# Performance work log

Measured on AMD Instinct MI355X. Metric: run time of the kernel, lower is better.

The kernel has to match this reference:

```python
import jax, jax.numpy as jnp
import numpy as np

B, N, DIM, H = 4, 1024, 384, 12
EPS = 1e-6


def setup_inputs() -> dict:
    key = jax.random.key(0)
    ks = jax.random.split(key, 5)
    return {
        "x": jax.random.normal(ks[0], (B, N, DIM), dtype=jnp.float32),
        "w_qkv": jax.random.normal(ks[1], (DIM, 3 * DIM), dtype=jnp.float32) * 0.05,
        "w_out": jax.random.normal(ks[2], (DIM, DIM), dtype=jnp.float32) * 0.05,
        "b_out": jax.random.normal(ks[3], (DIM,), dtype=jnp.float32) * 0.05,
        "toeplitz_w": jax.random.normal(ks[4], (2 * N - 1,), dtype=jnp.float32),
    }


def reference(x, w_qkv, w_out, b_out, toeplitz_w):
    b, n, c = x.shape
    d = c // H
    qkv = x @ w_qkv                                   # [B,N,3C]
    q, k, v = jnp.split(qkv, 3, axis=-1)
    def heads(t):
        return t.reshape(b, n, H, d).transpose(0, 2, 1, 3)  # [B,H,N,d]
    q, k, v = heads(q), heads(k), heads(v)
    q = jax.nn.relu(q) + EPS
    k = jax.nn.relu(k) + EPS
    # outer product kv signal: [B,H,N,d,d]
    kv = k[..., :, None] * v[..., None, :]
    kv_flat = kv.reshape(b * H, n, d * d)
    k_flat = k.reshape(b * H, n, d)
    combined = jnp.concatenate([kv_flat, k_flat], axis=-1)   # [BH,N,d^2+d]
    fft_len = 2 * n
    sig_f = jnp.fft.rfft(combined, n=fft_len, axis=1)        # [BH,N+1,d^2+d] complex
    w_pad = jnp.zeros(fft_len, dtype=x.dtype).at[: 2 * n - 1].set(toeplitz_w)
    w_rolled = jnp.roll(w_pad, -(n - 1))
    w_f = jnp.fft.rfft(w_rolled, n=fft_len)                  # [N+1]
    out_f = sig_f * w_f[None, :, None]
    out_t = jnp.fft.irfft(out_f, n=fft_len, axis=1)[:, :n, :]  # [BH,N,d^2+d]
    kv_conv = out_t[:, :, : d * d].reshape(b, H, n, d, d)
    k_conv = out_t[:, :, d * d:].reshape(b, H, n, d)
    num = jnp.einsum('bhnd,bhndc->bhnc', q, kv_conv)
    den = jnp.einsum('bhnd,bhnd->bhn', q, k_conv)[..., None] + EPS
    out = (num / den).transpose(0, 2, 1, 3).reshape(b, n, c)
    return out @ w_out.T + b_out
```

## Files before the change

kernel.cpp:

```cpp
#include <hip/hip_runtime.h>

#define EPS 1e-6f


__global__ __launch_bounds__(256) void qkv_gemm(const float* __restrict__ x,
                                                const float* __restrict__ w,
                                                float* __restrict__ qw,
                                                float* __restrict__ kw,
                                                float* __restrict__ vw) {
    __shared__ float As[16][132];
    __shared__ float Bs[16][128];
    const int t = threadIdx.x;
    const int m0 = blockIdx.y * 128;
    const int c0 = blockIdx.x * 128;
    const int tx = t & 15, ty = t >> 4;

    float acc[8][8];
#pragma unroll
    for (int i = 0; i < 8; i++)
#pragma unroll
        for (int j = 0; j < 8; j++) acc[i][j] = 0.f;

    for (int k0 = 0; k0 < 384; k0 += 16) {
        __syncthreads();
#pragma unroll
        for (int l = 0; l < 2; l++) {
            int idx = t * 2 + l;
            int r = idx >> 2, c4 = (idx & 3) * 4;
            float4 a = *(const float4*)(x + (size_t)(m0 + r) * 384 + k0 + c4);
            As[c4 + 0][r] = a.x;
            As[c4 + 1][r] = a.y;
            As[c4 + 2][r] = a.z;
            As[c4 + 3][r] = a.w;
        }
#pragma unroll
        for (int l = 0; l < 2; l++) {
            int idx = t * 2 + l;
            int kr = idx >> 5, cc = (idx & 31) * 4;
            *(float4*)&Bs[kr][cc] = *(const float4*)(w + (size_t)(k0 + kr) * 1152 + c0 + cc);
        }
        __syncthreads();
#pragma unroll
        for (int kk = 0; kk < 16; kk++) {
            float4 a0 = *(float4*)&As[kk][ty * 8];
            float4 a1 = *(float4*)&As[kk][ty * 8 + 4];
            float4 b0 = *(float4*)&Bs[kk][tx * 8];
            float4 b1 = *(float4*)&Bs[kk][tx * 8 + 4];
            float av[8] = {a0.x, a0.y, a0.z, a0.w, a1.x, a1.y, a1.z, a1.w};
            float bv[8] = {b0.x, b0.y, b0.z, b0.w, b1.x, b1.y, b1.z, b1.w};
#pragma unroll
            for (int i = 0; i < 8; i++)
#pragma unroll
                for (int j = 0; j < 8; j++) acc[i][j] += av[i] * bv[j];
        }
    }
#pragma unroll
    for (int i = 0; i < 8; i++) {
        int row = m0 + ty * 8 + i;
        int b = row >> 10, n = row & 1023;
#pragma unroll
        for (int j = 0; j < 8; j++) {
            int col = c0 + tx * 8 + j;
            float vv = acc[i][j];
            float* dst;
            int cc;
            if (col < 384) { dst = qw; cc = col; vv = fmaxf(vv, 0.f) + EPS; }
            else if (col < 768) { dst = kw; cc = col - 384; vv = fmaxf(vv, 0.f) + EPS; }
            else { dst = vw; cc = col - 768; }
            int h = cc >> 5, dd = cc & 31;
            dst[(size_t)((b * 12 + h) * 1024 + n) * 32 + dd] = vv;
        }
    }
}

__global__ __launch_bounds__(256) void toep_attn(const float* __restrict__ q,
                                                 const float* __restrict__ k,
                                                 const float* __restrict__ v,
                                                 const float* __restrict__ tw,
                                                 float* __restrict__ op) {
    const int t = threadIdx.x;
    const int n0 = blockIdx.x * 64;
    const int bh = blockIdx.y;
    const int b = bh / 12, h = bh % 12;
    __shared__ float Qt[32][68];
    __shared__ float Kt[32][68];
    __shared__ float Vs[64][32];
    __shared__ float Ss[64][68];
    __shared__ float Ts[128];

    const float* qb = q + (size_t)bh * 1024 * 32;
    const float* kb = k + (size_t)bh * 1024 * 32;
    const float* vb = v + (size_t)bh * 1024 * 32;

#pragma unroll
    for (int l = 0; l < 2; l++) {
        int idx = t * 2 + l;
        int r = idx >> 3, c4 = (idx & 7) * 4;
        float4 a = *(const float4*)(qb + (size_t)(n0 + r) * 32 + c4);
        Qt[c4 + 0][r] = a.x;
        Qt[c4 + 1][r] = a.y;
        Qt[c4 + 2][r] = a.z;
        Qt[c4 + 3][r] = a.w;
    }

    const int sx = t & 15, sy = t >> 4;
    const int pr = t >> 2;
    const int pc = (t & 3) * 8;
    double num[8] = {0, 0, 0, 0, 0, 0, 0, 0};
    double den = 0.0;

    for (int m0 = 0; m0 < 1024; m0 += 64) {
        __syncthreads();
#pragma unroll
        for (int l = 0; l < 2; l++) {
            int idx = t * 2 + l;
            int r = idx >> 3, c4 = (idx & 7) * 4;
            float4 a = *(const float4*)(kb + (size_t)(m0 + r) * 32 + c4);
            Kt[c4 + 0][r] = a.x;
            Kt[c4 + 1][r] = a.y;
            Kt[c4 + 2][r] = a.z;
            Kt[c4 + 3][r] = a.w;
            ((float4*)&Vs[0][0])[idx] = *(const float4*)(vb + (size_t)m0 * 32 + idx * 4);
        }
        if (t < 127) Ts[t] = tw[n0 - m0 + 960 + t];
        __syncthreads();

        float acc[4][4];
#pragma unroll
        for (int i = 0; i < 4; i++)
#pragma unroll
            for (int j = 0; j < 4; j++) acc[i][j] = 0.f;
#pragma unroll
        for (int kk = 0; kk < 32; kk++) {
            float4 a = *(float4*)&Qt[kk][sy * 4];
            float4 bb = *(float4*)&Kt[kk][sx * 4];
            float av[4] = {a.x, a.y, a.z, a.w};
            float bv[4] = {bb.x, bb.y, bb.z, bb.w};
#pragma unroll
            for (int i = 0; i < 4; i++)
#pragma unroll
                for (int j = 0; j < 4; j++) acc[i][j] += av[i] * bv[j];
        }
#pragma unroll
        for (int i = 0; i < 4; i++) {
            int r = sy * 4 + i;
            float4 srow;
            srow.x = acc[i][0] * Ts[r - sx * 4 + 63];
            srow.y = acc[i][1] * Ts[r - sx * 4 + 62];
            srow.z = acc[i][2] * Ts[r - sx * 4 + 61];
            srow.w = acc[i][3] * Ts[r - sx * 4 + 60];
            *(float4*)&Ss[r][sx * 4] = srow;
        }
        __syncthreads();

#pragma unroll 4
        for (int m = 0; m < 64; m++) {
            double s = (double)Ss[pr][m];
            float4 v0 = *(float4*)&Vs[m][pc];
            float4 v1 = *(float4*)&Vs[m][pc + 4];
            den += s;
            num[0] += s * (double)v0.x; num[1] += s * (double)v0.y;
            num[2] += s * (double)v0.z; num[3] += s * (double)v0.w;
            num[4] += s * (double)v1.x; num[5] += s * (double)v1.y;
            num[6] += s * (double)v1.z; num[7] += s * (double)v1.w;
        }
    }
    double inv = 1.0 / (den + (double)EPS);
    float* o = op + (size_t)((b * 1024) + n0 + pr) * 384 + h * 32 + pc;
    float4 o0 = {(float)(num[0] * inv), (float)(num[1] * inv),
                 (float)(num[2] * inv), (float)(num[3] * inv)};
    float4 o1 = {(float)(num[4] * inv), (float)(num[5] * inv),
                 (float)(num[6] * inv), (float)(num[7] * inv)};
    *(float4*)o = o0;
    *(float4*)(o + 4) = o1;
}

__global__ __launch_bounds__(256) void out_gemm(const float* __restrict__ a,
                                                const float* __restrict__ w,
                                                const float* __restrict__ bias,
                                                float* __restrict__ out) {
    __shared__ float As[16][132];
    __shared__ float Bs[16][132];
    const int t = threadIdx.x;
    const int m0 = blockIdx.y * 128;
    const int c0 = blockIdx.x * 128;
    const int tx = t & 15, ty = t >> 4;

    float acc[8][8];
#pragma unroll
    for (int i = 0; i < 8; i++)
#pragma unroll
        for (int j = 0; j < 8; j++) acc[i][j] = 0.f;

    for (int k0 = 0; k0 < 384; k0 += 16) {
        __syncthreads();
#pragma unroll
        for (int l = 0; l < 2; l++) {
            int idx = t * 2 + l;
            int r = idx >> 2, c4 = (idx & 3) * 4;
            float4 av = *(const float4*)(a + (size_t)(m0 + r) * 384 + k0 + c4);
            As[c4 + 0][r] = av.x;
            As[c4 + 1][r] = av.y;
            As[c4 + 2][r] = av.z;
            As[c4 + 3][r] = av.w;
        }
#pragma unroll
        for (int l = 0; l < 2; l++) {
            int idx = t * 2 + l;
            int r = idx >> 2, c4 = (idx & 3) * 4;
            float4 wv = *(const float4*)(w + (size_t)(c0 + r) * 384 + k0 + c4);
            Bs[c4 + 0][r] = wv.x;
            Bs[c4 + 1][r] = wv.y;
            Bs[c4 + 2][r] = wv.z;
            Bs[c4 + 3][r] = wv.w;
        }
        __syncthreads();
#pragma unroll
        for (int kk = 0; kk < 16; kk++) {
            float4 a0 = *(float4*)&As[kk][ty * 8];
            float4 a1 = *(float4*)&As[kk][ty * 8 + 4];
            float4 b0 = *(float4*)&Bs[kk][tx * 8];
            float4 b1 = *(float4*)&Bs[kk][tx * 8 + 4];
            float av[8] = {a0.x, a0.y, a0.z, a0.w, a1.x, a1.y, a1.z, a1.w};
            float bv[8] = {b0.x, b0.y, b0.z, b0.w, b1.x, b1.y, b1.z, b1.w};
#pragma unroll
            for (int i = 0; i < 8; i++)
#pragma unroll
                for (int j = 0; j < 8; j++) acc[i][j] += av[i] * bv[j];
        }
    }
#pragma unroll
    for (int i = 0; i < 8; i++) {
        int row = m0 + ty * 8 + i;
#pragma unroll
        for (int j = 0; j < 8; j++) {
            int col = c0 + tx * 8 + j;
            out[(size_t)row * 384 + col] = acc[i][j] + bias[col];
        }
    }
}

extern "C" void kernel_launch(void* const* d_in, const int* in_sizes, int n_in,
                              void* d_out, int out_size, void* d_ws, size_t ws_size,
                              hipStream_t stream) {
    const float* x     = (const float*)d_in[0];
    const float* w_qkv = (const float*)d_in[1];
    const float* w_out = (const float*)d_in[2];
    const float* b_out = (const float*)d_in[3];
    const float* tw    = (const float*)d_in[4];
    float* out = (float*)d_out;

    float* qw = (float*)d_ws;
    float* kw = qw + 1572864;
    float* vw = kw + 1572864;
    float* op = vw + 1572864;

    qkv_gemm<<<dim3(9, 32), 256, 0, stream>>>(x, w_qkv, qw, kw, vw);
    toep_attn<<<dim3(16, 48), 256, 0, stream>>>(qw, kw, vw, tw, op);
    out_gemm<<<dim3(3, 32), 256, 0, stream>>>(op, w_out, b_out, out);
}
```

Measured before the change: 367.2 us.

## Shrink GEMM tiles, vectorize epilogues, prefetch K/V and pre-convert V to double

```diff
diff --git a/kernel.cpp b/kernel.cpp
--- a/kernel.cpp
+++ b/kernel.cpp
@@ -8,25 +8,25 @@
                                                 float* __restrict__ qw,
                                                 float* __restrict__ kw,
                                                 float* __restrict__ vw) {
-    __shared__ float As[16][132];
-    __shared__ float Bs[16][128];
+    __shared__ float As[32][68];
+    __shared__ float Bs[32][68];
     const int t = threadIdx.x;
-    const int m0 = blockIdx.y * 128;
-    const int c0 = blockIdx.x * 128;
+    const int m0 = blockIdx.y * 64;
+    const int c0 = blockIdx.x * 64;
     const int tx = t & 15, ty = t >> 4;
 
-    float acc[8][8];
-#pragma unroll
-    for (int i = 0; i < 8; i++)
-#pragma unroll
-        for (int j = 0; j < 8; j++) acc[i][j] = 0.f;
-
-    for (int k0 = 0; k0 < 384; k0 += 16) {
+    float acc[4][4];
+#pragma unroll
+    for (int i = 0; i < 4; i++)
+#pragma unroll
+        for (int j = 0; j < 4; j++) acc[i][j] = 0.f;
+
+    for (int k0 = 0; k0 < 384; k0 += 32) {
         __syncthreads();
 #pragma unroll
         for (int l = 0; l < 2; l++) {
             int idx = t * 2 + l;
-            int r = idx >> 2, c4 = (idx & 3) * 4;
+            int r = idx >> 3, c4 = (idx & 7) * 4;
             float4 a = *(const float4*)(x + (size_t)(m0 + r) * 384 + k0 + c4);
             As[c4 + 0][r] = a.x;
             As[c4 + 1][r] = a.y;
@@ -36,40 +36,40 @@
 #pragma unroll
         for (int l = 0; l < 2; l++) {
             int idx = t * 2 + l;
-            int kr = idx >> 5, cc = (idx & 31) * 4;
+            int kr = idx >> 4, cc = (idx & 15) * 4;
             *(float4*)&Bs[kr][cc] = *(const float4*)(w + (size_t)(k0 + kr) * 1152 + c0 + cc);
         }
         __syncthreads();
 #pragma unroll
-        for (int kk = 0; kk < 16; kk++) {
-            float4 a0 = *(float4*)&As[kk][ty * 8];
-            float4 a1 = *(float4*)&As[kk][ty * 8 + 4];
-            float4 b0 = *(float4*)&Bs[kk][tx * 8];
-            float4 b1 = *(float4*)&Bs[kk][tx * 8 + 4];
-            float av[8] = {a0.x, a0.y, a0.z, a0.w, a1.x, a1.y, a1.z, a1.w};
-            float bv[8] = {b0.x, b0.y, b0.z, b0.w, b1.x, b1.y, b1.z, b1.w};
-#pragma unroll
-            for (int i = 0; i < 8; i++)
-#pragma unroll
-                for (int j = 0; j < 8; j++) acc[i][j] += av[i] * bv[j];
-        }
-    }
-#pragma unroll
-    for (int i = 0; i < 8; i++) {
-        int row = m0 + ty * 8 + i;
+        for (int kk = 0; kk < 32; kk++) {
+            float4 a = *(float4*)&As[kk][ty * 4];
+            float4 bb = *(float4*)&Bs[kk][tx * 4];
+            float av[4] = {a.x, a.y, a.z, a.w};
+            float bv[4] = {bb.x, bb.y, bb.z, bb.w};
+#pragma unroll
+            for (int i = 0; i < 4; i++)
+#pragma unroll
+                for (int j = 0; j < 4; j++) acc[i][j] += av[i] * bv[j];
+        }
+    }
+    const int sec = (c0 + tx * 4) / 384;
+    float* dst = (sec == 0) ? qw : (sec == 1) ? kw : vw;
+    const int cc0 = c0 + tx * 4 - sec * 384;
+    const int h = cc0 >> 5, dd = cc0 & 31;
+#pragma unroll
+    for (int i = 0; i < 4; i++) {
+        int row = m0 + ty * 4 + i;
         int b = row >> 10, n = row & 1023;
-#pragma unroll
-        for (int j = 0; j < 8; j++) {
-            int col = c0 + tx * 8 + j;
-            float vv = acc[i][j];
-            float* dst;
-            int cc;
-            if (col < 384) { dst = qw; cc = col; vv = fmaxf(vv, 0.f) + EPS; }
-            else if (col < 768) { dst = kw; cc = col - 384; vv = fmaxf(vv, 0.f) + EPS; }
-            else { dst = vw; cc = col - 768; }
-            int h = cc >> 5, dd = cc & 31;
-            dst[(size_t)((b * 12 + h) * 1024 + n) * 32 + dd] = vv;
-        }
+        float4 o;
+        if (sec < 2) {
+            o.x = fmaxf(acc[i][0], 0.f) + EPS;
+            o.y = fmaxf(acc[i][1], 0.f) + EPS;
+            o.z = fmaxf(acc[i][2], 0.f) + EPS;
+            o.w = fmaxf(acc[i][3], 0.f) + EPS;
+        } else {
+            o = make_float4(acc[i][0], acc[i][1], acc[i][2], acc[i][3]);
+        }
+        *(float4*)(dst + (size_t)((b * 12 + h) * 1024 + n) * 32 + dd) = o;
     }
 }
 
@@ -84,13 +84,13 @@
     const int b = bh / 12, h = bh % 12;
     __shared__ float Qt[32][68];
     __shared__ float Kt[32][68];
-    __shared__ float Vs[64][32];
+    __shared__ double Vd[64][32];
     __shared__ float Ss[64][68];
     __shared__ float Ts[128];
 
-    const float* qb = q + (size_t)bh * 1024 * 32;
-    const float* kb = k + (size_t)bh * 1024 * 32;
-    const float* vb = v + (size_t)bh * 1024 * 32;
+    const float* qb = q + (size_t)bh * 32768;
+    const float* kb = k + (size_t)bh * 32768;
+    const float* vb = v + (size_t)bh * 32768;
 
 #pragma unroll
     for (int l = 0; l < 2; l++) {
@@ -103,27 +103,47 @@
         Qt[c4 + 3][r] = a.w;
     }
 
+    float4 kreg[2], vreg[2];
+#pragma unroll
+    for (int l = 0; l < 2; l++) {
+        int idx = t * 2 + l;
+        int r = idx >> 3, c4 = (idx & 7) * 4;
+        kreg[l] = *(const float4*)(kb + (size_t)r * 32 + c4);
+        vreg[l] = *(const float4*)(vb + idx * 4);
+    }
+#pragma unroll
+    for (int l = 0; l < 2; l++) {
+        int idx = t * 2 + l;
+        int r = idx >> 3, c4 = (idx & 7) * 4;
+        Kt[c4 + 0][r] = kreg[l].x;
+        Kt[c4 + 1][r] = kreg[l].y;
+        Kt[c4 + 2][r] = kreg[l].z;
+        Kt[c4 + 3][r] = kreg[l].w;
+        double2 d0 = {(double)vreg[l].x, (double)vreg[l].y};
+        double2 d1 = {(double)vreg[l].z, (double)vreg[l].w};
+        *(double2*)&Vd[r][c4] = d0;
+        *(double2*)&Vd[r][c4 + 2] = d1;
+    }
+    if (t < 127) Ts[t] = tw[n0 + 960 + t];
+    __syncthreads();
+
     const int sx = t & 15, sy = t >> 4;
     const int pr = t >> 2;
     const int pc = (t & 3) * 8;
     double num[8] = {0, 0, 0, 0, 0, 0, 0, 0};
     double den = 0.0;
 
-    for (int m0 = 0; m0 < 1024; m0 += 64) {
-        __syncthreads();
-#pragma unroll
-        for (int l = 0; l < 2; l++) {
-            int idx = t * 2 + l;
-            int r = idx >> 3, c4 = (idx & 7) * 4;
-            float4 a = *(const float4*)(kb + (size_t)(m0 + r) * 32 + c4);
-            Kt[c4 + 0][r] = a.x;
-            Kt[c4 + 1][r] = a.y;
-            Kt[c4 + 2][r] = a.z;
-            Kt[c4 + 3][r] = a.w;
-            ((float4*)&Vs[0][0])[idx] = *(const float4*)(vb + (size_t)m0 * 32 + idx * 4);
-        }
-        if (t < 127) Ts[t] = tw[n0 - m0 + 960 + t];
-        __syncthreads();
+    for (int tt = 0; tt < 16; tt++) {
+        const int m0 = tt * 64;
+        if (tt < 15) {
+#pragma unroll
+            for (int l = 0; l < 2; l++) {
+                int idx = t * 2 + l;
+                int r = idx >> 3, c4 = (idx & 7) * 4;
+                kreg[l] = *(const float4*)(kb + (size_t)(m0 + 64 + r) * 32 + c4);
+                vreg[l] = *(const float4*)(vb + (size_t)(m0 + 64) * 32 + idx * 4);
+            }
+        }
 
         float acc[4][4];
 #pragma unroll
@@ -153,16 +173,43 @@
         }
         __syncthreads();
 
+        if (tt < 15) {
+#pragma unroll
+            for (int l = 0; l < 2; l++) {
+                int idx = t * 2 + l;
+                int r = idx >> 3, c4 = (idx & 7) * 4;
+                Kt[c4 + 0][r] = kreg[l].x;
+                Kt[c4 + 1][r] = kreg[l].y;
+                Kt[c4 + 2][r] = kreg[l].z;
+                Kt[c4 + 3][r] = kreg[l].w;
+            }
+            if (t < 127) Ts[t] = tw[n0 - (m0 + 64) + 960 + t];
+        }
+
 #pragma unroll 4
         for (int m = 0; m < 64; m++) {
             double s = (double)Ss[pr][m];
-            float4 v0 = *(float4*)&Vs[m][pc];
-            float4 v1 = *(float4*)&Vs[m][pc + 4];
+            double2 va = *(double2*)&Vd[m][pc];
+            double2 vb2 = *(double2*)&Vd[m][pc + 2];
+            double2 vc = *(double2*)&Vd[m][pc + 4];
+            double2 vd2 = *(double2*)&Vd[m][pc + 6];
             den += s;
-            num[0] += s * (double)v0.x; num[1] += s * (double)v0.y;
-            num[2] += s * (double)v0.z; num[3] += s * (double)v0.w;
-            num[4] += s * (double)v1.x; num[5] += s * (double)v1.y;
-            num[6] += s * (double)v1.z; num[7] += s * (double)v1.w;
+            num[0] += s * va.x;  num[1] += s * va.y;
+            num[2] += s * vb2.x; num[3] += s * vb2.y;
+            num[4] += s * vc.x;  num[5] += s * vc.y;
+            num[6] += s * vd2.x; num[7] += s * vd2.y;
+        }
+        __syncthreads();
+        if (tt < 15) {
+#pragma unroll
+            for (int l = 0; l < 2; l++) {
+                int idx = t * 2 + l;
+                int r = idx >> 3, c4 = (idx & 7) * 4;
+                double2 d0 = {(double)vreg[l].x, (double)vreg[l].y};
+                double2 d1 = {(double)vreg[l].z, (double)vreg[l].w};
+                *(double2*)&Vd[r][c4] = d0;
+                *(double2*)&Vd[r][c4 + 2] = d1;
+            }
         }
     }
     double inv = 1.0 / (den + (double)EPS);
@@ -179,25 +226,25 @@
                                                 const float* __restrict__ w,
                                                 const float* __restrict__ bias,
                                                 float* __restrict__ out) {
-    __shared__ float As[16][132];
-    __shared__ float Bs[16][132];
+    __shared__ float As[32][68];
+    __shared__ float Bs[32][68];
     const int t = threadIdx.x;
-    const int m0 = blockIdx.y * 128;
-    const int c0 = blockIdx.x * 128;
+    const int m0 = blockIdx.y * 64;
+    const int c0 = blockIdx.x * 64;
     const int tx = t & 15, ty = t >> 4;
 
-    float acc[8][8];
-#pragma unroll
-    for (int i = 0; i < 8; i++)
-#pragma unroll
-        for (int j = 0; j < 8; j++) acc[i][j] = 0.f;
-
-    for (int k0 = 0; k0 < 384; k0 += 16) {
+    float acc[4][4];
+#pragma unroll
+    for (int i = 0; i < 4; i++)
+#pragma unroll
+        for (int j = 0; j < 4; j++) acc[i][j] = 0.f;
+
+    for (int k0 = 0; k0 < 384; k0 += 32) {
         __syncthreads();
 #pragma unroll
         for (int l = 0; l < 2; l++) {
             int idx = t * 2 + l;
-            int r = idx >> 2, c4 = (idx & 3) * 4;
+            int r = idx >> 3, c4 = (idx & 7) * 4;
             float4 av = *(const float4*)(a + (size_t)(m0 + r) * 384 + k0 + c4);
             As[c4 + 0][r] = av.x;
             As[c4 + 1][r] = av.y;
@@ -207,7 +254,7 @@
 #pragma unroll
         for (int l = 0; l < 2; l++) {
             int idx = t * 2 + l;
-            int r = idx >> 2, c4 = (idx & 3) * 4;
+            int r = idx >> 3, c4 = (idx & 7) * 4;
             float4 wv = *(const float4*)(w + (size_t)(c0 + r) * 384 + k0 + c4);
             Bs[c4 + 0][r] = wv.x;
             Bs[c4 + 1][r] = wv.y;
@@ -216,27 +263,25 @@
         }
         __syncthreads();
 #pragma unroll
-        for (int kk = 0; kk < 16; kk++) {
-            float4 a0 = *(float4*)&As[kk][ty * 8];
-            float4 a1 = *(float4*)&As[kk][ty * 8 + 4];
-            float4 b0 = *(float4*)&Bs[kk][tx * 8];
-            float4 b1 = *(float4*)&Bs[kk][tx * 8 + 4];
-            float av[8] = {a0.x, a0.y, a0.z, a0.w, a1.x, a1.y, a1.z, a1.w};
-            float bv[8] = {b0.x, b0.y, b0.z, b0.w, b1.x, b1.y, b1.z, b1.w};
-#pragma unroll
-            for (int i = 0; i < 8; i++)
-#pragma unroll
-                for (int j = 0; j < 8; j++) acc[i][j] += av[i] * bv[j];
-        }
-    }
-#pragma unroll
-    for (int i = 0; i < 8; i++) {
-        int row = m0 + ty * 8 + i;
-#pragma unroll
-        for (int j = 0; j < 8; j++) {
-            int col = c0 + tx * 8 + j;
-            out[(size_t)row * 384 + col] = acc[i][j] + bias[col];
-        }
+        for (int kk = 0; kk < 32; kk++) {
+            float4 a4 = *(float4*)&As[kk][ty * 4];
+            float4 b4 = *(float4*)&Bs[kk][tx * 4];
+            float av[4] = {a4.x, a4.y, a4.z, a4.w};
+            float bv[4] = {b4.x, b4.y, b4.z, b4.w};
+#pragma unroll
+            for (int i = 0; i < 4; i++)
+#pragma unroll
+                for (int j = 0; j < 4; j++) acc[i][j] += av[i] * bv[j];
+        }
+    }
+    const int col = c0 + tx * 4;
+    float4 bb = *(const float4*)(bias + col);
+#pragma unroll
+    for (int i = 0; i < 4; i++) {
+        int row = m0 + ty * 4 + i;
+        float4 o = {acc[i][0] + bb.x, acc[i][1] + bb.y,
+                    acc[i][2] + bb.z, acc[i][3] + bb.w};
+        *(float4*)(out + (size_t)row * 384 + col) = o;
     }
 }
 
@@ -255,7 +300,7 @@
     float* vw = kw + 1572864;
     float* op = vw + 1572864;
 
-    qkv_gemm<<<dim3(9, 32), 256, 0, stream>>>(x, w_qkv, qw, kw, vw);
+    qkv_gemm<<<dim3(18, 64), 256, 0, stream>>>(x, w_qkv, qw, kw, vw);
     toep_attn<<<dim3(16, 48), 256, 0, stream>>>(qw, kw, vw, tw, op);
-    out_gemm<<<dim3(3, 32), 256, 0, stream>>>(op, w_out, b_out, out);
+    out_gemm<<<dim3(6, 64), 256, 0, stream>>>(op, w_out, b_out, out);
 }
```

New measurement: 323.0 us. 1.14x faster.
